# Optimization experiments

Measured on AMD Instinct MI355X. Metric: run time of the kernel, lower is better.

Reference implementation:

```python
import jax, jax.numpy as jnp
import numpy as np

MARGIN = 1.0


def _rand_offdiag(key, n):
    # uniform random index j != k for each row k (replaces Python random.choice)
    j = jax.random.randint(key, (n,), 0, n - 1)
    return j + (j >= jnp.arange(n)).astype(j.dtype)


def _semi_hard_margin_loss(logits, j_rand, j_fallback, margin):
    # logits: [N, N]; anchor for row k is logits[k, k]
    n = logits.shape[0]
    rows = jnp.arange(n)
    anchor = jnp.diagonal(logits)                      # [N]
    # term 1: random imposter, hinge at 0 (loss added only when diff > 0)
    imp1 = logits[rows, j_rand]
    d1 = jnp.maximum(imp1 - anchor + margin, 0.0)
    # term 2: semi-hard imposter = max over entries strictly below the anchor
    neg_inf = jnp.finfo(logits.dtype).min
    mask = logits < anchor[:, None]                    # diagonal never True
    cand_max = jnp.max(jnp.where(mask, logits, neg_inf), axis=1)
    has_cand = jnp.any(mask, axis=1)
    imp2 = jnp.where(has_cand, cand_max, logits[rows, j_fallback])
    d2 = jnp.maximum(imp2 - anchor + margin, 0.0)
    return jnp.mean(d1 + d2)


def setup_inputs() -> dict:
    key = jax.random.key(0)
    kx, ky = jax.random.split(key)
    x = jax.random.normal(kx, (4096, 1024), dtype=jnp.float32)
    y = jax.random.normal(ky, (4096, 1024), dtype=jnp.float32)
    return {"x": x, "y": y}


def reference(x, y):
    logits = jnp.matmul(x, y.T)                        # [N, N]
    n = logits.shape[0]
    k1, k2, k3, k4 = jax.random.split(jax.random.key(42), 4)
    loss = (_semi_hard_margin_loss(logits, _rand_offdiag(k1, n), _rand_offdiag(k2, n), MARGIN)
            + _semi_hard_margin_loss(logits.T, _rand_offdiag(k3, n), _rand_offdiag(k4, n), MARGIN))
    return loss
```

## Files before the change

### kernel.cpp

```cpp
#include <hip/hip_runtime.h>
#include <stdint.h>
#include <stddef.h>

#define NN 4096
#define KK 1024
#define SPAN 4095u

typedef unsigned short ushort_t;
typedef __attribute__((ext_vector_type(8))) short short8v;
typedef __attribute__((ext_vector_type(4))) float f32x4;

__host__ __device__ inline void tf2x32(uint32_t k0, uint32_t k1,
                                       uint32_t x0, uint32_t x1,
                                       uint32_t* o0, uint32_t* o1) {
  uint32_t ks2 = k0 ^ k1 ^ 0x1BD11BDAu;
  uint32_t v0 = x0 + k0;
  uint32_t v1 = x1 + k1;
#define TF_ROT(x, r) (((x) << (r)) | ((x) >> (32 - (r))))
#define TF_RND(r) do { v0 += v1; v1 = TF_ROT(v1, r); v1 ^= v0; } while (0)
  TF_RND(13); TF_RND(15); TF_RND(26); TF_RND(6);
  v0 += k1;  v1 += ks2 + 1u;
  TF_RND(17); TF_RND(29); TF_RND(16); TF_RND(24);
  v0 += ks2; v1 += k0 + 2u;
  TF_RND(13); TF_RND(15); TF_RND(26); TF_RND(6);
  v0 += k0;  v1 += k1 + 3u;
  TF_RND(17); TF_RND(29); TF_RND(16); TF_RND(24);
  v0 += k1;  v1 += ks2 + 4u;
  TF_RND(13); TF_RND(15); TF_RND(26); TF_RND(6);
  v0 += ks2; v1 += k0 + 5u;
#undef TF_RND
#undef TF_ROT
  *o0 = v0; *o1 = v1;
}

__device__ inline uint32_t rb32(uint32_t ka, uint32_t kb, uint32_t i) {
  uint32_t a, b;
  tf2x32(ka, kb, 0u, i, &a, &b);
  return a ^ b;
}

__device__ inline uint32_t fenc(float f) {
  uint32_t b = __float_as_uint(f);
  return (b & 0x80000000u) ? ~b : (b | 0x80000000u);
}
__device__ inline float fdec(uint32_t e) {
  uint32_t b = (e & 0x80000000u) ? (e & 0x7FFFFFFFu) : ~e;
  return __uint_as_float(b);
}

__device__ inline ushort_t bf16rne(float f) {
  uint32_t u = __float_as_uint(f);
  return (ushort_t)((u + 0x7FFFu + ((u >> 16) & 1u)) >> 16);
}

__device__ inline void glds16(const void* g, void* l) {
  __builtin_amdgcn_global_load_lds((const __attribute__((address_space(1))) void*)g,
                                   (__attribute__((address_space(3))) void*)l, 16, 0, 0);
}

__global__ __launch_bounds__(256) void k_prep(
    const float4* __restrict__ X, const float4* __restrict__ Y,
    ushort4* __restrict__ Xb, ushort4* __restrict__ Yb,
    uint32_t* __restrict__ rowmax, uint32_t* __restrict__ colmax) {
  const int b = blockIdx.x, tid = threadIdx.x;
  if (b < 16) rowmax[b * 256 + tid] = 0u;
  else if (b < 32) colmax[(b - 16) * 256 + tid] = 0u;
  const float4* src = (b < 2048) ? X : Y;
  ushort4* dst = (b < 2048) ? Xb : Yb;
  const int n4 = NN * KK / 4;
  for (int i = (b & 2047) * 256 + tid; i < n4; i += 2048 * 256) {
    float4 v = src[i];
    ushort4 o;
    o.x = bf16rne(v.x); o.y = bf16rne(v.y); o.z = bf16rne(v.z); o.w = bf16rne(v.w);
    dst[i] = o;
  }
}

__global__ __launch_bounds__(256) void k_dots(
    const float* __restrict__ X, const float* __restrict__ Y,
    uint32_t s0a, uint32_t s0b, uint32_t s1a, uint32_t s1b,
    uint32_t s2a, uint32_t s2b, uint32_t s3a, uint32_t s3b,
    float* __restrict__ anchor, float* __restrict__ irr, float* __restrict__ irf,
    float* __restrict__ icr, float* __restrict__ icf) {
  const int wid = threadIdx.x >> 6;
  const int lane = threadIdx.x & 63;
  const int row = blockIdx.x * 4 + wid;

  int jl = 0;
  if (lane < 4) {
    uint32_t ka = (lane == 0) ? s0a : (lane == 1) ? s1a : (lane == 2) ? s2a : s3a;
    uint32_t kb = (lane == 0) ? s0b : (lane == 1) ? s1b : (lane == 2) ? s2b : s3b;
    uint32_t k1a, k1b, k2a, k2b;
    tf2x32(ka, kb, 0u, 0u, &k1a, &k1b);
    tf2x32(ka, kb, 0u, 1u, &k2a, &k2b);
    uint32_t hi = rb32(k1a, k1b, (uint32_t)row);
    uint32_t lo = rb32(k2a, k2b, (uint32_t)row);
    uint32_t off = ((hi % SPAN) * 256u + (lo % SPAN)) % SPAN;
    int j = (int)off;
    jl = j + ((j >= row) ? 1 : 0);
  }
  const int j1r = __shfl(jl, 0), j1f = __shfl(jl, 1);
  const int j2r = __shfl(jl, 2), j2f = __shfl(jl, 3);

  const float4* xk = (const float4*)(X + (size_t)row * KK);
  const float4* yk = (const float4*)(Y + (size_t)row * KK);
  const float4* y1 = (const float4*)(Y + (size_t)j1r * KK);
  const float4* y2 = (const float4*)(Y + (size_t)j1f * KK);
  const float4* x1 = (const float4*)(X + (size_t)j2r * KK);
  const float4* x2 = (const float4*)(X + (size_t)j2f * KK);
  float sa = 0.f, s1 = 0.f, s2 = 0.f, s3 = 0.f, s4 = 0.f;
  for (int t = lane; t < KK / 4; t += 64) {
    float4 xv = xk[t], yv = yk[t], a1 = y1[t], a2 = y2[t], b1 = x1[t], b2 = x2[t];
    sa = fmaf(xv.x, yv.x, fmaf(xv.y, yv.y, fmaf(xv.z, yv.z, fmaf(xv.w, yv.w, sa))));
    s1 = fmaf(xv.x, a1.x, fmaf(xv.y, a1.y, fmaf(xv.z, a1.z, fmaf(xv.w, a1.w, s1))));
    s2 = fmaf(xv.x, a2.x, fmaf(xv.y, a2.y, fmaf(xv.z, a2.z, fmaf(xv.w, a2.w, s2))));
    s3 = fmaf(b1.x, yv.x, fmaf(b1.y, yv.y, fmaf(b1.z, yv.z, fmaf(b1.w, yv.w, s3))));
    s4 = fmaf(b2.x, yv.x, fmaf(b2.y, yv.y, fmaf(b2.z, yv.z, fmaf(b2.w, yv.w, s4))));
  }
  for (int m = 32; m >= 1; m >>= 1) {
    sa += __shfl_xor(sa, m);
    s1 += __shfl_xor(s1, m);
    s2 += __shfl_xor(s2, m);
    s3 += __shfl_xor(s3, m);
    s4 += __shfl_xor(s4, m);
  }
  if (lane == 0) {
    anchor[row] = sa; irr[row] = s1; irf[row] = s2; icr[row] = s3; icf[row] = s4;
  }
}


__global__ __launch_bounds__(512, 2) void k_gemm8p(
    const ushort_t* __restrict__ A, const ushort_t* __restrict__ B,
    const float* __restrict__ anchor,
    uint32_t* __restrict__ rowmax, uint32_t* __restrict__ colmax) {
  __shared__ ushort_t AL[2][2][8192];
  __shared__ ushort_t BL[2][2][8192];

  const int tid = threadIdx.x;
  const int lane = tid & 63;
  const int w = tid >> 6, wr = w >> 2, wc = w & 3;
  const int l15 = lane & 15, l4 = lane >> 4;

  const int swz = (blockIdx.x & 7) * 32 + (blockIdx.x >> 3);
  const int bi = swz >> 4, bj = swz & 15;

  const int strow = tid >> 3;
  const int scol = ((tid & 7) ^ (strow & 7)) * 8;
  const ushort_t* Abase = A + (size_t)(bi * 256 + strow) * KK + scol;
  const ushort_t* Bbase = B + (size_t)(bj * 256 + strow) * KK + scol;

  const int ss0 = ((0 * 4 + l4) ^ (l15 & 7)) * 8;
  const int ss1 = ((1 * 4 + l4) ^ (l15 & 7)) * 8;
  const int bhalf = wc >> 1, brow0 = (wc & 1) * 64 + l15;

  f32x4 acc[8][4] = {};
  short8v Areg[4][2], B0r[2][2], B1r[2][2];

#define STAGE_A(DD, KT)                                                        \
  do {                                                                         \
    glds16(Abase + (size_t)0 * KK + (KT) * 64,   &AL[DD][0][tid * 8]);         \
    glds16(Abase + (size_t)64 * KK + (KT) * 64,  &AL[DD][0][4096 + tid * 8]);  \
    glds16(Abase + (size_t)128 * KK + (KT) * 64, &AL[DD][1][tid * 8]);         \
    glds16(Abase + (size_t)192 * KK + (KT) * 64, &AL[DD][1][4096 + tid * 8]);  \
  } while (0)
#define STAGE_B(DD, KT)                                                        \
  do {                                                                         \
    glds16(Bbase + (size_t)0 * KK + (KT) * 64,   &BL[DD][0][tid * 8]);         \
    glds16(Bbase + (size_t)64 * KK + (KT) * 64,  &BL[DD][0][4096 + tid * 8]);  \
    glds16(Bbase + (size_t)128 * KK + (KT) * 64, &BL[DD][1][tid * 8]);         \
    glds16(Bbase + (size_t)192 * KK + (KT) * 64, &BL[DD][1][4096 + tid * 8]);  \
  } while (0)

#define BAR() do { __builtin_amdgcn_s_barrier(); \
                   __builtin_amdgcn_sched_barrier(0); } while (0)
#define LGKM0() do { asm volatile("s_waitcnt lgkmcnt(0)" ::: "memory"); \
                     __builtin_amdgcn_sched_barrier(0); } while (0)
#define VM8BAR() do { asm volatile("s_waitcnt vmcnt(8)" ::: "memory"); \
                      __builtin_amdgcn_s_barrier(); \
                      __builtin_amdgcn_sched_barrier(0); } while (0)

#define MFMA1(a, b, c) c = __builtin_amdgcn_mfma_f32_16x16x32_bf16(a, b, c, 0, 0, 0)
#define CL16(MS, NS, BR)                                                       \
  do {                                                                         \
    __builtin_amdgcn_s_setprio(1);                                             \
    _Pragma("unroll")                                                          \
    for (int q = 0; q < 4; ++q) {                                              \
      MFMA1(Areg[q][0], BR[0][0], acc[(MS) * 4 + q][(NS) * 2]);                \
      MFMA1(Areg[q][0], BR[1][0], acc[(MS) * 4 + q][(NS) * 2 + 1]);            \
      MFMA1(Areg[q][1], BR[0][1], acc[(MS) * 4 + q][(NS) * 2]);                \
      MFMA1(Areg[q][1], BR[1][1], acc[(MS) * 4 + q][(NS) * 2 + 1]);            \
    }                                                                          \
    __builtin_amdgcn_s_setprio(0);                                             \
  } while (0)

#define LDA(D, M, KH) (*(const short8v*)&AL[D][wr][((M) * 16 + l15) * 64 + ((KH) ? ss1 : ss0)])
#define LDB(D, N, KH) (*(const short8v*)&BL[D][bhalf][(brow0 + (N) * 16) * 64 + ((KH) ? ss1 : ss0)])

  STAGE_B(0, 0); STAGE_A(0, 0);
  STAGE_B(1, 1); STAGE_A(1, 1);
  asm volatile("s_waitcnt vmcnt(8)" ::: "memory");
  __builtin_amdgcn_s_barrier();
  __builtin_amdgcn_sched_barrier(0);

  for (int i = 0; i < 8; ++i) {
    const int kt2 = (2 * i + 2) & 15, kt3 = (2 * i + 3) & 15;

#pragma unroll
    for (int q = 0; q < 4; ++q) { Areg[q][0] = LDA(0, q, 0); Areg[q][1] = LDA(0, q, 1); }
#pragma unroll
    for (int n = 0; n < 2; ++n) { B0r[n][0] = LDB(0, n, 0); B0r[n][1] = LDB(0, n, 1); }
    BAR(); LGKM0();
    CL16(0, 0, B0r);
    BAR();

#pragma unroll
    for (int n = 0; n < 2; ++n) { B1r[n][0] = LDB(0, n + 2, 0); B1r[n][1] = LDB(0, n + 2, 1); }
    BAR(); LGKM0();
    CL16(0, 1, B1r);
    BAR();

#pragma unroll
    for (int q = 0; q < 4; ++q) { Areg[q][0] = LDA(0, q + 4, 0); Areg[q][1] = LDA(0, q + 4, 1); }
    STAGE_B(0, kt2);
    BAR(); LGKM0();
    CL16(1, 1, B1r);
    BAR();

    STAGE_A(0, kt2);
    BAR(); LGKM0();
    CL16(1, 0, B0r);
    VM8BAR();

#pragma unroll
    for (int q = 0; q < 4; ++q) { Areg[q][0] = LDA(1, q, 0); Areg[q][1] = LDA(1, q, 1); }
#pragma unroll
    for (int n = 0; n < 2; ++n) { B0r[n][0] = LDB(1, n, 0); B0r[n][1] = LDB(1, n, 1); }
    BAR(); LGKM0();
    CL16(0, 0, B0r);
    BAR();

#pragma unroll
    for (int n = 0; n < 2; ++n) { B1r[n][0] = LDB(1, n + 2, 0); B1r[n][1] = LDB(1, n + 2, 1); }
    BAR(); LGKM0();
    CL16(0, 1, B1r);
    BAR();

#pragma unroll
    for (int q = 0; q < 4; ++q) { Areg[q][0] = LDA(1, q + 4, 0); Areg[q][1] = LDA(1, q + 4, 1); }
    STAGE_B(1, kt3);
    BAR(); LGKM0();
    CL16(1, 1, B1r);
    BAR();

    STAGE_A(1, kt3);
    BAR(); LGKM0();
    CL16(1, 0, B0r);
    VM8BAR();
  }

#undef LDA
#undef LDB
#undef CL16
#undef MFMA1
#undef VM8BAR
#undef LGKM0
#undef BAR
#undef STAGE_A
#undef STAGE_B

  const int rbase = bi * 256 + wr * 128;
  const int cbase = bj * 256 + wc * 64;

  float ar[32], ac[4];
#pragma unroll
  for (int m = 0; m < 8; ++m)
#pragma unroll
    for (int r = 0; r < 4; ++r)
      ar[m * 4 + r] = anchor[rbase + m * 16 + l4 * 4 + r];
#pragma unroll
  for (int n = 0; n < 4; ++n)
    ac[n] = anchor[cbase + n * 16 + l15];

#pragma unroll
  for (int m = 0; m < 8; ++m) {
#pragma unroll
    for (int r = 0; r < 4; ++r) {
      const int rg = rbase + m * 16 + l4 * 4 + r;
      const float a = ar[m * 4 + r];
      uint32_t e = 0;
#pragma unroll
      for (int n = 0; n < 4; ++n) {
        const int cg = cbase + n * 16 + l15;
        float v = acc[m][n][r];
        if (v < a && rg != cg) { uint32_t fe = fenc(v); e = (fe > e) ? fe : e; }
      }
#pragma unroll
      for (int sh = 1; sh < 16; sh <<= 1) {
        uint32_t o = (uint32_t)__shfl_xor((int)e, sh, 64);
        e = (o > e) ? o : e;
      }
      if (l15 == 0 && e) atomicMax(&rowmax[rg], e);
    }
  }
#pragma unroll
  for (int n = 0; n < 4; ++n) {
    const int cg = cbase + n * 16 + l15;
    const float a = ac[n];
    uint32_t e = 0;
#pragma unroll
    for (int m = 0; m < 8; ++m) {
#pragma unroll
      for (int r = 0; r < 4; ++r) {
        const int rg = rbase + m * 16 + l4 * 4 + r;
        float v = acc[m][n][r];
        if (v < a && rg != cg) { uint32_t fe = fenc(v); e = (fe > e) ? fe : e; }
      }
    }
    {
      uint32_t o = (uint32_t)__shfl_xor((int)e, 16, 64); e = (o > e) ? o : e;
      o = (uint32_t)__shfl_xor((int)e, 32, 64);          e = (o > e) ? o : e;
    }
    if (l4 == 0 && e) atomicMax(&colmax[cg], e);
  }
}

__global__ __launch_bounds__(256) void k_final(
    const float* __restrict__ anchor,
    const float* __restrict__ irr, const float* __restrict__ irf,
    const float* __restrict__ icr, const float* __restrict__ icf,
    const uint32_t* __restrict__ rowmax, const uint32_t* __restrict__ colmax,
    float* __restrict__ out) {
  float s = 0.f;
  for (int k = (int)threadIdx.x; k < NN; k += 256) {
    float a = anchor[k];
    float d1 = fmaxf(irr[k] - a + 1.0f, 0.f);
    uint32_t rm = rowmax[k];
    float imp2r = rm ? fdec(rm) : irf[k];
    float d2 = fmaxf(imp2r - a + 1.0f, 0.f);
    float e1 = fmaxf(icr[k] - a + 1.0f, 0.f);
    uint32_t cm = colmax[k];
    float imp2c = cm ? fdec(cm) : icf[k];
    float e2 = fmaxf(imp2c - a + 1.0f, 0.f);
    s += d1 + d2 + e1 + e2;
  }
  __shared__ float red[4];
  for (int m = 32; m >= 1; m >>= 1) s += __shfl_xor(s, m);
  if ((threadIdx.x & 63) == 0) red[threadIdx.x >> 6] = s;
  __syncthreads();
  if (threadIdx.x == 0) out[0] = (red[0] + red[1] + red[2] + red[3]) * (1.0f / NN);
}

extern "C" void kernel_launch(void* const* d_in, const int* in_sizes, int n_in,
                              void* d_out, int out_size, void* d_ws, size_t ws_size,
                              hipStream_t stream) {
  const float* X = (const float*)d_in[0];
  const float* Y = (const float*)d_in[1];
  float* out = (float*)d_out;

  char* ws = (char*)d_ws;
  float* anchor    = (float*)(ws + 0 * 16384);
  float* irr       = (float*)(ws + 1 * 16384);
  float* irf       = (float*)(ws + 2 * 16384);
  float* icr       = (float*)(ws + 3 * 16384);
  float* icf       = (float*)(ws + 4 * 16384);
  uint32_t* rowmax = (uint32_t*)(ws + 5 * 16384);
  uint32_t* colmax = (uint32_t*)(ws + 6 * 16384);
  ushort_t* Xb     = (ushort_t*)(ws + 256 * 1024);
  ushort_t* Yb     = Xb + (size_t)NN * KK;

  uint32_t sk[4][2];
  for (int i = 0; i < 4; ++i) tf2x32(0u, 42u, 0u, (uint32_t)i, &sk[i][0], &sk[i][1]);

  k_prep<<<4096, 256, 0, stream>>>((const float4*)X, (const float4*)Y,
                                   (ushort4*)Xb, (ushort4*)Yb, rowmax, colmax);

  k_dots<<<NN / 4, 256, 0, stream>>>(X, Y,
      sk[0][0], sk[0][1], sk[1][0], sk[1][1], sk[2][0], sk[2][1], sk[3][0], sk[3][1],
      anchor, irr, irf, icr, icf);

  k_gemm8p<<<256, 512, 0, stream>>>(Xb, Yb, anchor, rowmax, colmax);

  k_final<<<1, 256, 0, stream>>>(anchor, irr, irf, icr, icf, rowmax, colmax, out);
}
```

Baseline: 94.77 us.

## Restructure GEMM main loop schedule and compute dots from bf16 copies

The GEMM inner loop is rewritten to iterate over all 16 k-tiles with a new register double-buffering scheme. A-fragments are split by k-half with all four B fragments held per step, and the global-to-LDS staging and waitcnt placement are reordered. The dot-product kernel now reads the bf16 copies instead of the fp32 inputs, which halves its memory traffic. The bf16 dots also keep the anchor consistent with the bf16 GEMM used for the mask comparisons, at the cost of reduced precision for the hinge terms.

```diff
diff --git a/kernel.cpp b/kernel.cpp
--- a/kernel.cpp
+++ b/kernel.cpp
@@ -52,6 +52,9 @@
   uint32_t u = __float_as_uint(f);
   return (ushort_t)((u + 0x7FFFu + ((u >> 16) & 1u)) >> 16);
 }
+__device__ inline float bf2f(ushort_t v) {
+  return __uint_as_float(((uint32_t)v) << 16);
+}
 
 __device__ inline void glds16(const void* g, void* l) {
   __builtin_amdgcn_global_load_lds((const __attribute__((address_space(1))) void*)g,
@@ -77,7 +80,7 @@
 }
 
 __global__ __launch_bounds__(256) void k_dots(
-    const float* __restrict__ X, const float* __restrict__ Y,
+    const ushort_t* __restrict__ Xb, const ushort_t* __restrict__ Yb,
     uint32_t s0a, uint32_t s0b, uint32_t s1a, uint32_t s1b,
     uint32_t s2a, uint32_t s2b, uint32_t s3a, uint32_t s3b,
     float* __restrict__ anchor, float* __restrict__ irr, float* __restrict__ irf,
@@ -102,20 +105,24 @@
   const int j1r = __shfl(jl, 0), j1f = __shfl(jl, 1);
   const int j2r = __shfl(jl, 2), j2f = __shfl(jl, 3);
 
-  const float4* xk = (const float4*)(X + (size_t)row * KK);
-  const float4* yk = (const float4*)(Y + (size_t)row * KK);
-  const float4* y1 = (const float4*)(Y + (size_t)j1r * KK);
-  const float4* y2 = (const float4*)(Y + (size_t)j1f * KK);
-  const float4* x1 = (const float4*)(X + (size_t)j2r * KK);
-  const float4* x2 = (const float4*)(X + (size_t)j2f * KK);
+  const short8v* xk = (const short8v*)(Xb + (size_t)row * KK);
+  const short8v* yk = (const short8v*)(Yb + (size_t)row * KK);
+  const short8v* y1 = (const short8v*)(Yb + (size_t)j1r * KK);
+  const short8v* y2 = (const short8v*)(Yb + (size_t)j1f * KK);
+  const short8v* x1 = (const short8v*)(Xb + (size_t)j2r * KK);
+  const short8v* x2 = (const short8v*)(Xb + (size_t)j2f * KK);
   float sa = 0.f, s1 = 0.f, s2 = 0.f, s3 = 0.f, s4 = 0.f;
-  for (int t = lane; t < KK / 4; t += 64) {
-    float4 xv = xk[t], yv = yk[t], a1 = y1[t], a2 = y2[t], b1 = x1[t], b2 = x2[t];
-    sa = fmaf(xv.x, yv.x, fmaf(xv.y, yv.y, fmaf(xv.z, yv.z, fmaf(xv.w, yv.w, sa))));
-    s1 = fmaf(xv.x, a1.x, fmaf(xv.y, a1.y, fmaf(xv.z, a1.z, fmaf(xv.w, a1.w, s1))));
-    s2 = fmaf(xv.x, a2.x, fmaf(xv.y, a2.y, fmaf(xv.z, a2.z, fmaf(xv.w, a2.w, s2))));
-    s3 = fmaf(b1.x, yv.x, fmaf(b1.y, yv.y, fmaf(b1.z, yv.z, fmaf(b1.w, yv.w, s3))));
-    s4 = fmaf(b2.x, yv.x, fmaf(b2.y, yv.y, fmaf(b2.z, yv.z, fmaf(b2.w, yv.w, s4))));
+  for (int t = lane; t < KK / 8; t += 64) {
+    short8v xv = xk[t], yv = yk[t], a1 = y1[t], a2 = y2[t], b1 = x1[t], b2 = x2[t];
+#pragma unroll
+    for (int j = 0; j < 8; ++j) {
+      float xf = bf2f((ushort_t)xv[j]), yf = bf2f((ushort_t)yv[j]);
+      sa = fmaf(xf, yf, sa);
+      s1 = fmaf(xf, bf2f((ushort_t)a1[j]), s1);
+      s2 = fmaf(xf, bf2f((ushort_t)a2[j]), s2);
+      s3 = fmaf(bf2f((ushort_t)b1[j]), yf, s3);
+      s4 = fmaf(bf2f((ushort_t)b2[j]), yf, s4);
+    }
   }
   for (int m = 32; m >= 1; m >>= 1) {
     sa += __shfl_xor(sa, m);
@@ -130,7 +137,7 @@
 }
 
 
-__global__ __launch_bounds__(512, 2) void k_gemm8p(
+__global__ __launch_bounds__(512, 2) void k_gemm_xp(
     const ushort_t* __restrict__ A, const ushort_t* __restrict__ B,
     const float* __restrict__ anchor,
     uint32_t* __restrict__ rowmax, uint32_t* __restrict__ colmax) {
@@ -155,7 +162,7 @@
   const int bhalf = wc >> 1, brow0 = (wc & 1) * 64 + l15;
 
   f32x4 acc[8][4] = {};
-  short8v Areg[4][2], B0r[2][2], B1r[2][2];
+  short8v aR[2][4], bR[2][4];
 
 #define STAGE_A(DD, KT)                                                        \
   do {                                                                         \
@@ -172,102 +179,82 @@
     glds16(Bbase + (size_t)192 * KK + (KT) * 64, &BL[DD][1][4096 + tid * 8]);  \
   } while (0)
 
-#define BAR() do { __builtin_amdgcn_s_barrier(); \
-                   __builtin_amdgcn_sched_barrier(0); } while (0)
-#define LGKM0() do { asm volatile("s_waitcnt lgkmcnt(0)" ::: "memory"); \
-                     __builtin_amdgcn_sched_barrier(0); } while (0)
-#define VM8BAR() do { asm volatile("s_waitcnt vmcnt(8)" ::: "memory"); \
-                      __builtin_amdgcn_s_barrier(); \
-                      __builtin_amdgcn_sched_barrier(0); } while (0)
+#define RD_A(S, D, MH, KH)                                                     \
+  do {                                                                         \
+    _Pragma("unroll")                                                          \
+    for (int q = 0; q < 4; ++q)                                                \
+      aR[S][q] = *(const short8v*)&AL[D][wr][(((MH) * 4 + q) * 16 + l15) * 64  \
+                                             + ((KH) ? ss1 : ss0)];            \
+  } while (0)
+#define RD_B(S, D, KH)                                                         \
+  do {                                                                         \
+    _Pragma("unroll")                                                          \
+    for (int n = 0; n < 4; ++n)                                                \
+      bR[S][n] = *(const short8v*)&BL[D][bhalf][(brow0 + n * 16) * 64          \
+                                                + ((KH) ? ss1 : ss0)];         \
+  } while (0)
 
 #define MFMA1(a, b, c) c = __builtin_amdgcn_mfma_f32_16x16x32_bf16(a, b, c, 0, 0, 0)
-#define CL16(MS, NS, BR)                                                       \
+#define CL16(AS, BS, MH)                                                       \
   do {                                                                         \
     __builtin_amdgcn_s_setprio(1);                                             \
     _Pragma("unroll")                                                          \
     for (int q = 0; q < 4; ++q) {                                              \
-      MFMA1(Areg[q][0], BR[0][0], acc[(MS) * 4 + q][(NS) * 2]);                \
-      MFMA1(Areg[q][0], BR[1][0], acc[(MS) * 4 + q][(NS) * 2 + 1]);            \
-      MFMA1(Areg[q][1], BR[0][1], acc[(MS) * 4 + q][(NS) * 2]);                \
-      MFMA1(Areg[q][1], BR[1][1], acc[(MS) * 4 + q][(NS) * 2 + 1]);            \
+      MFMA1(aR[AS][q], bR[BS][0], acc[(MH) * 4 + q][0]);                       \
+      MFMA1(aR[AS][q], bR[BS][1], acc[(MH) * 4 + q][1]);                       \
+      MFMA1(aR[AS][q], bR[BS][2], acc[(MH) * 4 + q][2]);                       \
+      MFMA1(aR[AS][q], bR[BS][3], acc[(MH) * 4 + q][3]);                       \
     }                                                                          \
     __builtin_amdgcn_s_setprio(0);                                             \
   } while (0)
 
-#define LDA(D, M, KH) (*(const short8v*)&AL[D][wr][((M) * 16 + l15) * 64 + ((KH) ? ss1 : ss0)])
-#define LDB(D, N, KH) (*(const short8v*)&BL[D][bhalf][(brow0 + (N) * 16) * 64 + ((KH) ? ss1 : ss0)])
-
-  STAGE_B(0, 0); STAGE_A(0, 0);
-  STAGE_B(1, 1); STAGE_A(1, 1);
-  asm volatile("s_waitcnt vmcnt(8)" ::: "memory");
-  __builtin_amdgcn_s_barrier();
-  __builtin_amdgcn_sched_barrier(0);
-
-  for (int i = 0; i < 8; ++i) {
-    const int kt2 = (2 * i + 2) & 15, kt3 = (2 * i + 3) & 15;
-
-#pragma unroll
-    for (int q = 0; q < 4; ++q) { Areg[q][0] = LDA(0, q, 0); Areg[q][1] = LDA(0, q, 1); }
-#pragma unroll
-    for (int n = 0; n < 2; ++n) { B0r[n][0] = LDB(0, n, 0); B0r[n][1] = LDB(0, n, 1); }
-    BAR(); LGKM0();
-    CL16(0, 0, B0r);
-    BAR();
-
-#pragma unroll
-    for (int n = 0; n < 2; ++n) { B1r[n][0] = LDB(0, n + 2, 0); B1r[n][1] = LDB(0, n + 2, 1); }
-    BAR(); LGKM0();
-    CL16(0, 1, B1r);
-    BAR();
-
-#pragma unroll
-    for (int q = 0; q < 4; ++q) { Areg[q][0] = LDA(0, q + 4, 0); Areg[q][1] = LDA(0, q + 4, 1); }
-    STAGE_B(0, kt2);
-    BAR(); LGKM0();
-    CL16(1, 1, B1r);
-    BAR();
-
-    STAGE_A(0, kt2);
-    BAR(); LGKM0();
-    CL16(1, 0, B0r);
-    VM8BAR();
-
-#pragma unroll
-    for (int q = 0; q < 4; ++q) { Areg[q][0] = LDA(1, q, 0); Areg[q][1] = LDA(1, q, 1); }
-#pragma unroll
-    for (int n = 0; n < 2; ++n) { B0r[n][0] = LDB(1, n, 0); B0r[n][1] = LDB(1, n, 1); }
-    BAR(); LGKM0();
-    CL16(0, 0, B0r);
-    BAR();
-
-#pragma unroll
-    for (int n = 0; n < 2; ++n) { B1r[n][0] = LDB(1, n + 2, 0); B1r[n][1] = LDB(1, n + 2, 1); }
-    BAR(); LGKM0();
-    CL16(0, 1, B1r);
-    BAR();
-
-#pragma unroll
-    for (int q = 0; q < 4; ++q) { Areg[q][0] = LDA(1, q + 4, 0); Areg[q][1] = LDA(1, q + 4, 1); }
-    STAGE_B(1, kt3);
-    BAR(); LGKM0();
-    CL16(1, 1, B1r);
-    BAR();
-
-    STAGE_A(1, kt3);
-    BAR(); LGKM0();
-    CL16(1, 0, B0r);
-    VM8BAR();
-  }
-
-#undef LDA
-#undef LDB
+#define BAR() __builtin_amdgcn_s_barrier()
+#define VM0() asm volatile("s_waitcnt vmcnt(0)" ::: "memory")
+#define VM4() asm volatile("s_waitcnt vmcnt(4)" ::: "memory")
+
+  STAGE_A(0, 0); STAGE_B(0, 0); STAGE_B(1, 1);
+  VM4();
+  BAR();
+  RD_A(0, 0, 0, 0);
+  RD_B(0, 0, 0);
+
+  for (int u = 0; u < 16; ++u) {
+    const int d = u & 1, dn = d ^ 1;
+
+    if (u < 15) STAGE_A(dn, u + 1);
+    RD_A(1, d, 1, 0);
+    BAR();
+    CL16(0, 0, 0);
+    BAR();
+
+    RD_A(0, d, 0, 1);
+    RD_B(1, d, 1);
+    BAR();
+    CL16(1, 0, 1);
+    BAR();
+
+    RD_A(1, d, 1, 1);
+    BAR();
+    CL16(0, 1, 0);
+    VM0();
+    BAR();
+
+    if (u < 15) { RD_A(0, dn, 0, 0); RD_B(0, dn, 0); }
+    if (u < 14) STAGE_B(d, u + 2);
+    BAR();
+    CL16(1, 1, 1);
+    BAR();
+  }
+
+#undef VM4
+#undef VM0
+#undef BAR
 #undef CL16
 #undef MFMA1
-#undef VM8BAR
-#undef LGKM0
-#undef BAR
+#undef RD_B
+#undef RD_A
+#undef STAGE_B
 #undef STAGE_A
-#undef STAGE_B
 
   const int rbase = bi * 256 + wr * 128;
   const int cbase = bj * 256 + wc * 64;
@@ -375,11 +362,11 @@
   k_prep<<<4096, 256, 0, stream>>>((const float4*)X, (const float4*)Y,
                                    (ushort4*)Xb, (ushort4*)Yb, rowmax, colmax);
 
-  k_dots<<<NN / 4, 256, 0, stream>>>(X, Y,
+  k_dots<<<NN / 4, 256, 0, stream>>>(Xb, Yb,
       sk[0][0], sk[0][1], sk[1][0], sk[1][1], sk[2][0], sk[2][1], sk[3][0], sk[3][1],
       anchor, irr, irf, icr, icf);
 
-  k_gemm8p<<<256, 512, 0, stream>>>(Xb, Yb, anchor, rowmax, colmax);
+  k_gemm_xp<<<256, 512, 0, stream>>>(Xb, Yb, anchor, rowmax, colmax);
 
   k_final<<<1, 256, 0, stream>>>(anchor, irr, irf, icr, icf, rowmax, colmax, out);
 }
```

Result: no change. 93.63 us (-1.2%).
